# Optimization experiments

Hardware: AMD Instinct MI355X
Metric: run time of the kernel (lower is better)

The kernel has to match this reference:

```python
import jax, jax.numpy as jnp
import numpy as np

DIM = 3072
NUM_HEADS = 24
HEAD_DIM = 128
EPS = 1e-6


def setup_inputs() -> dict:
    key = jax.random.key(0)
    ks = jax.random.split(key, 16)
    B, S_new, S_cached = 2, 256, 8192
    s = 0.02
    return {
        "x": jax.random.normal(ks[0], (B, S_new, DIM), jnp.float32),
        "freqs": jax.random.uniform(ks[1], (S_new, HEAD_DIM // 2), jnp.float32, 0.0, 2 * np.pi),
        "k_cache": jax.random.normal(ks[2], (B, S_cached, DIM), jnp.float32),
        "v_cache": jax.random.normal(ks[3], (B, S_cached, DIM), jnp.float32),
        "Wq": jax.random.normal(ks[4], (DIM, DIM), jnp.float32) * s,
        "bq": jnp.zeros((DIM,), jnp.float32),
        "Wk": jax.random.normal(ks[5], (DIM, DIM), jnp.float32) * s,
        "bk": jnp.zeros((DIM,), jnp.float32),
        "Wv": jax.random.normal(ks[6], (DIM, DIM), jnp.float32) * s,
        "bv": jnp.zeros((DIM,), jnp.float32),
        "Wo": jax.random.normal(ks[7], (DIM, DIM), jnp.float32) * s,
        "bo": jnp.zeros((DIM,), jnp.float32),
        "gq": jnp.ones((DIM,), jnp.float32),
        "gk": jnp.ones((DIM,), jnp.float32),
    }


def _rmsnorm(t, g):
    return t * jax.lax.rsqrt(jnp.mean(t * t, axis=-1, keepdims=True) + EPS) * g


def _rope(t, freqs):
    # t: [B, S, DIM]; freqs: [S, HEAD_DIM//2] angles (complex e^{i*theta} multiply,
    # interleaved-pair layout, matching torch view_as_complex on (..., d//2, 2)).
    B, S, D = t.shape
    th = t.reshape(B, S, NUM_HEADS, HEAD_DIM // 2, 2)
    c = jnp.cos(freqs)[None, :, None, :]
    s = jnp.sin(freqs)[None, :, None, :]
    re = th[..., 0] * c - th[..., 1] * s
    im = th[..., 0] * s + th[..., 1] * c
    return jnp.stack([re, im], axis=-1).reshape(B, S, D)


def reference(x, freqs, k_cache, v_cache, Wq, bq, Wk, bk, Wv, bv, Wo, bo, gq, gk):
    B, S_new, _ = x.shape
    S_cached = k_cache.shape[1]
    S_tot = S_cached + S_new

    q = _rmsnorm(x @ Wq.T + bq, gq)
    k = _rmsnorm(x @ Wk.T + bk, gk)
    v = x @ Wv.T + bv

    q = _rope(q, freqs)
    k = _rope(k, freqs)

    # 'extend' cache mode: concat cached K/V with new K/V
    full_k = jnp.concatenate([k_cache, k], axis=1)
    full_v = jnp.concatenate([v_cache, v], axis=1)

    qh = q.reshape(B, S_new, NUM_HEADS, HEAD_DIM)
    kh = full_k.reshape(B, S_tot, NUM_HEADS, HEAD_DIM)
    vh = full_v.reshape(B, S_tot, NUM_HEADS, HEAD_DIM)

    scale = 1.0 / np.sqrt(HEAD_DIM)
    scores = jnp.einsum("bqhd,bkhd->bhqk", qh, kh) * scale
    probs = jax.nn.softmax(scores, axis=-1)
    out = jnp.einsum("bhqk,bkhd->bqhd", probs, vh).reshape(B, S_new, DIM)
    return out @ Wo.T + bo
```

## Files before the change

kernel.cpp:

```cpp
#include <hip/hip_runtime.h>
#include <hip/hip_bf16.h>

#define NH 24
#define HD 128
#define DM 3072
#define NB 2
#define SN 256
#define MR 512
#define SCACHE 8192
#define NCH 9

typedef float f32x4 __attribute__((ext_vector_type(4)));
typedef float f32x2 __attribute__((ext_vector_type(2)));
typedef short s16x8 __attribute__((ext_vector_type(8)));
typedef short s16x4 __attribute__((ext_vector_type(4)));
typedef unsigned u32x4 __attribute__((ext_vector_type(4)));

__device__ __forceinline__ short bfc(float f) {
    __hip_bfloat16 h = __float2bfloat16(f);
    return __builtin_bit_cast(short, h);
}

__global__ __launch_bounds__(256) void xcast(const float* __restrict__ src, short* __restrict__ dst)
{
    const int i = (blockIdx.x * 256 + threadIdx.x) * 8;
    f32x4 a = *(const f32x4*)(src + i);
    f32x4 b = *(const f32x4*)(src + i + 4);
    s16x8 o;
    #pragma unroll
    for (int j = 0; j < 4; ++j) { o[j] = bfc(a[j]); o[4 + j] = bfc(b[j]); }
    *(s16x8*)(dst + i) = o;
}

__global__ __launch_bounds__(256, 3) void gemm_bias(
    const short* __restrict__ A,
    const float* __restrict__ W0, const float* __restrict__ W1, const float* __restrict__ W2,
    const float* __restrict__ b0, const float* __restrict__ b1, const float* __restrict__ b2,
    float* __restrict__ O0, float* __restrict__ O1, float* __restrict__ O2)
{
    const int z = blockIdx.z;
    const float* W    = (z == 0) ? W0 : (z == 1) ? W1 : W2;
    const float* bias = (z == 0) ? b0 : (z == 1) ? b1 : b2;
    float* O          = (z == 0) ? O0 : (z == 1) ? O1 : O2;

    const int n0 = blockIdx.x * 64;
    const int m0 = blockIdx.y * 128;
    const int t = threadIdx.x;
    const int lane = t & 63;
    const int wave = t >> 6;
    const int l15 = lane & 15, l4 = lane >> 4;
    const int wm = wave * 32;

    __shared__ short As[128][72];
    __shared__ short Bs[64][72];

    f32x4 acc[2][4] = {};
    s16x8 areg[4];
    f32x4 breg[4];

    #pragma unroll
    for (int i = 0; i < 4; ++i) {
        int lin = i * 256 + t;
        areg[i] = *(const s16x8*)(A + (size_t)(m0 + (lin >> 3)) * DM + (lin & 7) * 8);
    }
    #pragma unroll
    for (int i = 0; i < 4; ++i) {
        int lin = i * 256 + t;
        breg[i] = *(const f32x4*)(W + (size_t)(n0 + (lin >> 4)) * DM + (lin & 15) * 4);
    }

    for (int ks = 0; ks < DM / 64; ++ks) {
        #pragma unroll
        for (int i = 0; i < 4; ++i) {
            int lin = i * 256 + t;
            *(s16x8*)&As[lin >> 3][(lin & 7) * 8] = areg[i];
        }
        #pragma unroll
        for (int i = 0; i < 4; ++i) {
            int lin = i * 256 + t;
            s16x4 w4;
            #pragma unroll
            for (int j = 0; j < 4; ++j) w4[j] = bfc(breg[i][j]);
            *(s16x4*)&Bs[lin >> 4][(lin & 15) * 4] = w4;
        }
        __syncthreads();
        if (ks + 1 < DM / 64) {
            int k0 = (ks + 1) * 64;
            #pragma unroll
            for (int i = 0; i < 4; ++i) {
                int lin = i * 256 + t;
                areg[i] = *(const s16x8*)(A + (size_t)(m0 + (lin >> 3)) * DM + k0 + (lin & 7) * 8);
            }
            #pragma unroll
            for (int i = 0; i < 4; ++i) {
                int lin = i * 256 + t;
                breg[i] = *(const f32x4*)(W + (size_t)(n0 + (lin >> 4)) * DM + k0 + (lin & 15) * 4);
            }
        }
        #pragma unroll
        for (int kt = 0; kt < 2; ++kt) {
            s16x8 af[2], bfr[4];
            #pragma unroll
            for (int i = 0; i < 2; ++i)
                af[i]  = *(const s16x8*)&As[wm + i * 16 + l15][kt * 32 + l4 * 8];
            #pragma unroll
            for (int i = 0; i < 4; ++i)
                bfr[i] = *(const s16x8*)&Bs[i * 16 + l15][kt * 32 + l4 * 8];
            #pragma unroll
            for (int mi = 0; mi < 2; ++mi)
                #pragma unroll
                for (int ni = 0; ni < 4; ++ni)
                    acc[mi][ni] = __builtin_amdgcn_mfma_f32_16x16x32_bf16(
                        af[mi], bfr[ni], acc[mi][ni], 0, 0, 0);
        }
        __syncthreads();
    }

    #pragma unroll
    for (int ni = 0; ni < 4; ++ni) {
        int col = n0 + ni * 16 + l15;
        float bv = bias[col];
        #pragma unroll
        for (int mi = 0; mi < 2; ++mi) {
            int row = m0 + wm + mi * 16 + l4 * 4;
            #pragma unroll
            for (int r = 0; r < 4; ++r)
                O[(size_t)(row + r) * DM + col] = acc[mi][ni][r] + bv;
        }
    }
}

__global__ __launch_bounds__(256) void norm_rope(
    float* __restrict__ qf, float* __restrict__ kf, short* __restrict__ qbf,
    const float* __restrict__ gq, const float* __restrict__ gk,
    const float* __restrict__ freqs)
{
    const int buf = blockIdx.x >> 9;
    const int row = blockIdx.x & 511;
    const int t = threadIdx.x;
    float* src = buf ? kf : qf;
    const float* g = buf ? gk : gq;

    f32x2 v[6];
    float ss = 0.f;
    #pragma unroll
    for (int i = 0; i < 6; ++i) {
        int p = t + 256 * i;
        v[i] = *(const f32x2*)(src + (size_t)row * DM + 2 * p);
        ss += v[i][0] * v[i][0] + v[i][1] * v[i][1];
    }
    #pragma unroll
    for (int m = 1; m < 64; m <<= 1) ss += __shfl_xor(ss, m);
    __shared__ float red[4];
    if ((t & 63) == 0) red[t >> 6] = ss;
    __syncthreads();
    ss = red[0] + red[1] + red[2] + red[3];
    const float scale = rsqrtf(ss * (1.0f / DM) + 1e-6f);
    const float QS = 0.08838834764831845f * 1.4426950408889634f;

    const int spos = row & 255;
    #pragma unroll
    for (int i = 0; i < 6; ++i) {
        int p = t + 256 * i;
        int d2 = p & 63;
        float fr = freqs[spos * 64 + d2];
        float snv, cs;
        __sincosf(fr, &snv, &cs);
        f32x2 gg = *(const f32x2*)(g + 2 * p);
        float re = v[i][0] * scale * gg[0];
        float im = v[i][1] * scale * gg[1];
        float re2 = re * cs - im * snv;
        float im2 = re * snv + im * cs;
        if (buf == 0) {
            re2 *= QS; im2 *= QS;
            unsigned pack = (unsigned)(unsigned short)bfc(re2)
                          | ((unsigned)(unsigned short)bfc(im2) << 16);
            *(unsigned*)(qbf + (size_t)row * DM + 2 * p) = pack;
        } else {
            f32x2 o; o[0] = re2; o[1] = im2;
            *(f32x2*)(src + (size_t)row * DM + 2 * p) = o;
        }
    }
}

__global__ __launch_bounds__(512) void attn_fa(
    const short* __restrict__ qbf,
    const float* __restrict__ kf, const float* __restrict__ vf,
    const float* __restrict__ kcache, const float* __restrict__ vcache,
    short* __restrict__ partO, float* __restrict__ partM, float* __restrict__ partL)
{
    const int bid = blockIdx.x;
    const int linear = (bid & 7) * 54 + (bid >> 3);
    const int c  = linear / 48;
    const int bh = linear % 48;
    const int b = bh / NH, h = bh % NH;
    const int t = threadIdx.x, lane = t & 63, wave = t >> 6;
    const int l15 = lane & 15, l4 = lane >> 4;
    const int hoff = h * HD;

    __shared__ short KsA[2][64 * 128];
    __shared__ short VtA[2][128 * 64];

    s16x8 qb[2][4];
    #pragma unroll
    for (int nj = 0; nj < 2; ++nj) {
        int qrow = b * SN + wave * 32 + nj * 16 + l15;
        #pragma unroll
        for (int kt = 0; kt < 4; ++kt)
            qb[nj][kt] = *(const s16x8*)(qbf + (size_t)qrow * DM + hoff + kt * 32 + l4 * 8);
    }

    f32x4 acc[2][8] = {};
    float mrun[2] = {-INFINITY, -INFINITY};
    float lpart[2] = {0.f, 0.f};

    const int ts = (c < 6) ? c * 15 : 90 + (c - 6) * 14;
    const int NT = (c < 6) ? 15 : 14;

    const float* kcB = kcache + (size_t)b * SCACHE * DM + hoff;
    const float* knB = kf     + (size_t)b * SN * DM + hoff;
    const float* vcB = vcache + (size_t)b * SCACHE * DM + hoff;
    const float* vnB = vf     + (size_t)b * SN * DM + hoff;

    auto kaddr = [&](int r, int col) -> const float* {
        return (r < SCACHE) ? (kcB + (size_t)r * DM + col)
                            : (knB + (size_t)(r - SCACHE) * DM + col);
    };
    auto vaddr = [&](int r, int col) -> const float* {
        return (r < SCACHE) ? (vcB + (size_t)r * DM + col)
                            : (vnB + (size_t)(r - SCACHE) * DM + col);
    };

    const int vrow = t & 63, vw = t >> 6;
    f32x4 kreg[4], vreg[4];

    {
        const int kr = ts * 64;
        #pragma unroll
        for (int i = 0; i < 4; ++i) {
            int lin = i * 512 + t;
            kreg[i] = *(const f32x4*)kaddr(kr + (lin >> 5), (lin & 31) * 4);
        }
        #pragma unroll
        for (int j = 0; j < 4; ++j)
            vreg[j] = *(const f32x4*)vaddr(kr + vrow, vw * 16 + j * 4);
    }

    const bool ghi = (l4 & 2) != 0;
    const bool gin = (l4 == 0) || (l4 == 3);

    for (int nt = 0; nt < NT; ++nt) {
        char* KsB = (char*)KsA[nt & 1];
        char* VtB = (char*)VtA[nt & 1];

        #pragma unroll
        for (int i = 0; i < 4; ++i) {
            int lin = i * 512 + t;
            int row = lin >> 5, col4 = lin & 31;
            s16x4 k4;
            #pragma unroll
            for (int j = 0; j < 4; ++j) k4[j] = bfc(kreg[i][j]);
            *(s16x4*)(KsB + (row << 8) + ((((col4 >> 1) ^ row) & 15) << 4) + ((col4 & 1) << 3)) = k4;
        }
        #pragma unroll
        for (int j = 0; j < 4; ++j) {
            #pragma unroll
            for (int jj = 0; jj < 4; ++jj) {
                int d = vw * 16 + j * 4 + jj;
                *(short*)(VtB + (d << 7) + ((((vrow >> 3) ^ (d & 7))) << 4) + ((vrow & 7) << 1)) = bfc(vreg[j][jj]);
            }
        }
        __syncthreads();

        if (nt + 1 < NT) {
            const int kr1 = (ts + nt + 1) * 64;
            #pragma unroll
            for (int i = 0; i < 4; ++i) {
                int lin = i * 512 + t;
                kreg[i] = *(const f32x4*)kaddr(kr1 + (lin >> 5), (lin & 31) * 4);
            }
            #pragma unroll
            for (int j = 0; j < 4; ++j)
                vreg[j] = *(const f32x4*)vaddr(kr1 + vrow, vw * 16 + j * 4);
        }

        f32x4 st[4][2] = {};
        #pragma unroll
        for (int kt = 0; kt < 4; ++kt)
            #pragma unroll
            for (int mi = 0; mi < 4; ++mi) {
                int row = mi * 16 + l15;
                s16x8 kfr = *(const s16x8*)(KsB + (row << 8) + (((kt * 4 + l4) ^ l15) << 4));
                st[mi][0] = __builtin_amdgcn_mfma_f32_16x16x32_bf16(kfr, qb[0][kt], st[mi][0], 0, 0, 0);
                st[mi][1] = __builtin_amdgcn_mfma_f32_16x16x32_bf16(kfr, qb[1][kt], st[mi][1], 0, 0, 0);
            }

        float lx0 = fmaxf(
            fmaxf(fmaxf(fmaxf(st[0][0][0], st[0][0][1]), fmaxf(st[0][0][2], st[0][0][3])),
                  fmaxf(fmaxf(st[1][0][0], st[1][0][1]), fmaxf(st[1][0][2], st[1][0][3]))),
            fmaxf(fmaxf(fmaxf(st[2][0][0], st[2][0][1]), fmaxf(st[2][0][2], st[2][0][3])),
                  fmaxf(fmaxf(st[3][0][0], st[3][0][1]), fmaxf(st[3][0][2], st[3][0][3]))));
        float lx1 = fmaxf(
            fmaxf(fmaxf(fmaxf(st[0][1][0], st[0][1][1]), fmaxf(st[0][1][2], st[0][1][3])),
                  fmaxf(fmaxf(st[1][1][0], st[1][1][1]), fmaxf(st[1][1][2], st[1][1][3]))),
            fmaxf(fmaxf(fmaxf(st[2][1][0], st[2][1][1]), fmaxf(st[2][1][2], st[2][1][3])),
                  fmaxf(fmaxf(st[3][1][0], st[3][1][1]), fmaxf(st[3][1][2], st[3][1][3]))));

        if (!__all((lx0 <= mrun[0] + 8.0f) && (lx1 <= mrun[1] + 8.0f))) {
            float lm0 = fmaxf(lx0, __shfl_xor(lx0, 16)); lm0 = fmaxf(lm0, __shfl_xor(lm0, 32));
            float lm1 = fmaxf(lx1, __shfl_xor(lx1, 16)); lm1 = fmaxf(lm1, __shfl_xor(lm1, 32));
            float mn0 = fmaxf(mrun[0], lm0), mn1 = fmaxf(mrun[1], lm1);
            float c0 = exp2f(mrun[0] - mn0), c1 = exp2f(mrun[1] - mn1);
            mrun[0] = mn0; mrun[1] = mn1;
            lpart[0] *= c0; lpart[1] *= c1;
            #pragma unroll
            for (int df = 0; df < 8; ++df) { acc[0][df] *= c0; acc[1][df] *= c1; }
        }

        #pragma unroll
        for (int mi = 0; mi < 4; ++mi)
            #pragma unroll
            for (int r = 0; r < 4; ++r) {
                float p0 = exp2f(st[mi][0][r] - mrun[0]);
                float p1 = exp2f(st[mi][1][r] - mrun[1]);
                st[mi][0][r] = p0; st[mi][1][r] = p1;
                lpart[0] += p0; lpart[1] += p1;
            }

        unsigned up[2][4][2];
        #pragma unroll
        for (int nj = 0; nj < 2; ++nj)
            #pragma unroll
            for (int mi = 0; mi < 4; ++mi)
                #pragma unroll
                for (int i = 0; i < 2; ++i)
                    up[nj][mi][i] = (unsigned)(unsigned short)bfc(st[mi][nj][2 * i])
                                  | ((unsigned)(unsigned short)bfc(st[mi][nj][2 * i + 1]) << 16);

        s16x8 bp[2][2];
        #pragma unroll
        for (int nj = 0; nj < 2; ++nj)
            #pragma unroll
            for (int kt2 = 0; kt2 < 2; ++kt2) {
                unsigned own0 = ghi ? up[nj][kt2 * 2 + 1][0] : up[nj][kt2 * 2 + 0][0];
                unsigned own1 = ghi ? up[nj][kt2 * 2 + 1][1] : up[nj][kt2 * 2 + 0][1];
                unsigned alt0 = ghi ? up[nj][kt2 * 2 + 0][0] : up[nj][kt2 * 2 + 1][0];
                unsigned alt1 = ghi ? up[nj][kt2 * 2 + 0][1] : up[nj][kt2 * 2 + 1][1];
                unsigned o16_0 = __shfl_xor(own0, 16), o16_1 = __shfl_xor(own1, 16);
                unsigned o32_0 = __shfl_xor(alt0, 32), o32_1 = __shfl_xor(alt1, 32);
                unsigned o48_0 = __shfl_xor(alt0, 48), o48_1 = __shfl_xor(alt1, 48);
                u32x4 uu;
                uu[0] = gin ? (ghi ? o16_0 : own0) : (ghi ? o32_0 : o48_0);
                uu[1] = gin ? (ghi ? o16_1 : own1) : (ghi ? o32_1 : o48_1);
                uu[2] = gin ? (ghi ? own0 : o16_0) : (ghi ? o48_0 : o32_0);
                uu[3] = gin ? (ghi ? own1 : o16_1) : (ghi ? o48_1 : o32_1);
                bp[nj][kt2] = __builtin_bit_cast(s16x8, uu);
            }

        #pragma unroll
        for (int kt2 = 0; kt2 < 2; ++kt2)
            #pragma unroll
            for (int df = 0; df < 8; ++df) {
                int row = df * 16 + l15;
                s16x8 vfr = *(const s16x8*)(VtB + (row << 7) + (((kt2 * 4 + l4) ^ (row & 7)) << 4));
                acc[0][df] = __builtin_amdgcn_mfma_f32_16x16x32_bf16(vfr, bp[0][kt2], acc[0][df], 0, 0, 0);
                acc[1][df] = __builtin_amdgcn_mfma_f32_16x16x32_bf16(vfr, bp[1][kt2], acc[1][df], 0, 0, 0);
            }
    }

    float l0 = lpart[0]; l0 += __shfl_xor(l0, 16); l0 += __shfl_xor(l0, 32);
    float l1 = lpart[1]; l1 += __shfl_xor(l1, 16); l1 += __shfl_xor(l1, 32);

    #pragma unroll
    for (int nj = 0; nj < 2; ++nj) {
        size_t rowid = (size_t)bh * SN + wave * 32 + nj * 16 + l15;
        short* po = partO + (rowid * NCH + c) * HD + l4 * 4;
        #pragma unroll
        for (int df = 0; df < 8; ++df) {
            s16x4 ob;
            #pragma unroll
            for (int r = 0; r < 4; ++r) ob[r] = bfc(acc[nj][df][r]);
            *(s16x4*)(po + df * 16) = ob;
        }
        if (l4 == 0) {
            partM[rowid * NCH + c] = mrun[nj];
            partL[rowid * NCH + c] = (nj == 0) ? l0 : l1;
        }
    }
}

__global__ __launch_bounds__(128) void combine(
    const short* __restrict__ partO, const float* __restrict__ partM,
    const float* __restrict__ partL, short* __restrict__ attnb)
{
    const int rowid = blockIdx.x;
    const int bh = rowid >> 8, q = rowid & 255;
    const int b = bh / NH, h = bh % NH;
    const int d = threadIdx.x;

    float m[NCH];
    float M = -INFINITY;
    #pragma unroll
    for (int c = 0; c < NCH; ++c) { m[c] = partM[(size_t)rowid * NCH + c]; M = fmaxf(M, m[c]); }
    float L = 0.f, o = 0.f;
    #pragma unroll
    for (int c = 0; c < NCH; ++c) {
        float w = exp2f(m[c] - M);
        L += partL[(size_t)rowid * NCH + c] * w;
        unsigned ub = (unsigned)(unsigned short)partO[((size_t)rowid * NCH + c) * HD + d];
        float ov = __builtin_bit_cast(float, ub << 16);
        o += ov * w;
    }
    attnb[(size_t)(b * SN + q) * DM + h * HD + d] = bfc(o / L);
}

extern "C" void kernel_launch(void* const* d_in, const int* in_sizes, int n_in,
                              void* d_out, int out_size, void* d_ws, size_t ws_size,
                              hipStream_t stream) {
    const float* x      = (const float*)d_in[0];
    const float* freqs  = (const float*)d_in[1];
    const float* kcache = (const float*)d_in[2];
    const float* vcache = (const float*)d_in[3];
    const float* Wq = (const float*)d_in[4];
    const float* bq = (const float*)d_in[5];
    const float* Wk = (const float*)d_in[6];
    const float* bk = (const float*)d_in[7];
    const float* Wv = (const float*)d_in[8];
    const float* bv = (const float*)d_in[9];
    const float* Wo = (const float*)d_in[10];
    const float* bo = (const float*)d_in[11];
    const float* gq = (const float*)d_in[12];
    const float* gk = (const float*)d_in[13];
    float* out = (float*)d_out;

    auto al = [](size_t v) { return (v + 255) & ~(size_t)255; };
    const size_t SZ_QF  = (size_t)MR * DM * 4;
    const size_t SZ_QBF = (size_t)MR * DM * 2;
    const size_t SZ_PML = (size_t)48 * SN * NCH * 4;
    const size_t SZ_PO  = (size_t)48 * SN * NCH * HD * 2;

    char* ws = (char*)d_ws;
    float* qf    = (float*)ws; ws += al(SZ_QF);
    float* kfb   = (float*)ws; ws += al(SZ_QF);
    float* vfb   = (float*)ws; ws += al(SZ_QF);
    short* qbf   = (short*)ws; ws += al(SZ_QBF);
    short* xb    = (short*)ws; ws += al(SZ_QBF);
    short* attnb = (short*)ws; ws += al(SZ_QBF);
    float* pM    = (float*)ws; ws += al(SZ_PML);
    float* pL    = (float*)ws; ws += al(SZ_PML);
    short* pO    = (short*)ws; ws += al(SZ_PO);

    xcast<<<dim3(768), 256, 0, stream>>>(x, xb);
    gemm_bias<<<dim3(48, 4, 3), 256, 0, stream>>>(xb, Wq, Wk, Wv, bq, bk, bv, qf, kfb, vfb);
    norm_rope<<<dim3(1024), 256, 0, stream>>>(qf, kfb, qbf, gq, gk, freqs);
    attn_fa<<<dim3(432), 512, 0, stream>>>(qbf, kfb, vfb, kcache, vcache, pO, pM, pL);
    combine<<<dim3(12288), 128, 0, stream>>>(pO, pM, pL, attnb);
    gemm_bias<<<dim3(48, 4, 1), 256, 0, stream>>>(attnb, Wo, Wo, Wo, bo, bo, bo, out, out, out);
}
```

Before: 275.0 us.

## Compute softmax row sums with MFMA against ones and hoist K/V tile base selection

Result: no change. 273.4 us (median of 2 runs) (-0.6%).

```diff
diff --git a/kernel.cpp b/kernel.cpp
--- a/kernel.cpp
+++ b/kernel.cpp
@@ -183,7 +183,7 @@
     }
 }
 
-__global__ __launch_bounds__(512) void attn_fa(
+__global__ __launch_bounds__(512, 2) void attn_fa(
     const short* __restrict__ qbf,
     const float* __restrict__ kf, const float* __restrict__ vf,
     const float* __restrict__ kcache, const float* __restrict__ vcache,
@@ -211,8 +211,12 @@
     }
 
     f32x4 acc[2][8] = {};
+    f32x4 accL[2] = {};
     float mrun[2] = {-INFINITY, -INFINITY};
-    float lpart[2] = {0.f, 0.f};
+
+    s16x8 ones1;
+    #pragma unroll
+    for (int j = 0; j < 8; ++j) ones1[j] = (short)0x3F80;
 
     const int ts = (c < 6) ? c * 15 : 90 + (c - 6) * 14;
     const int NT = (c < 6) ? 15 : 14;
@@ -222,28 +226,22 @@
     const float* vcB = vcache + (size_t)b * SCACHE * DM + hoff;
     const float* vnB = vf     + (size_t)b * SN * DM + hoff;
 
-    auto kaddr = [&](int r, int col) -> const float* {
-        return (r < SCACHE) ? (kcB + (size_t)r * DM + col)
-                            : (knB + (size_t)(r - SCACHE) * DM + col);
-    };
-    auto vaddr = [&](int r, int col) -> const float* {
-        return (r < SCACHE) ? (vcB + (size_t)r * DM + col)
-                            : (vnB + (size_t)(r - SCACHE) * DM + col);
-    };
-
     const int vrow = t & 63, vw = t >> 6;
     f32x4 kreg[4], vreg[4];
 
     {
         const int kr = ts * 64;
+        const float* kb; const float* vb;
+        if (kr < SCACHE) { kb = kcB + (size_t)kr * DM; vb = vcB + (size_t)kr * DM; }
+        else             { kb = knB + (size_t)(kr - SCACHE) * DM; vb = vnB + (size_t)(kr - SCACHE) * DM; }
         #pragma unroll
         for (int i = 0; i < 4; ++i) {
             int lin = i * 512 + t;
-            kreg[i] = *(const f32x4*)kaddr(kr + (lin >> 5), (lin & 31) * 4);
+            kreg[i] = *(const f32x4*)(kb + (size_t)(lin >> 5) * DM + (lin & 31) * 4);
         }
         #pragma unroll
         for (int j = 0; j < 4; ++j)
-            vreg[j] = *(const f32x4*)vaddr(kr + vrow, vw * 16 + j * 4);
+            vreg[j] = *(const f32x4*)(vb + (size_t)vrow * DM + vw * 16 + j * 4);
     }
 
     const bool ghi = (l4 & 2) != 0;
@@ -274,14 +272,17 @@
 
         if (nt + 1 < NT) {
             const int kr1 = (ts + nt + 1) * 64;
+            const float* kb; const float* vb;
+            if (kr1 < SCACHE) { kb = kcB + (size_t)kr1 * DM; vb = vcB + (size_t)kr1 * DM; }
+            else              { kb = knB + (size_t)(kr1 - SCACHE) * DM; vb = vnB + (size_t)(kr1 - SCACHE) * DM; }
             #pragma unroll
             for (int i = 0; i < 4; ++i) {
                 int lin = i * 512 + t;
-                kreg[i] = *(const f32x4*)kaddr(kr1 + (lin >> 5), (lin & 31) * 4);
+                kreg[i] = *(const f32x4*)(kb + (size_t)(lin >> 5) * DM + (lin & 31) * 4);
             }
             #pragma unroll
             for (int j = 0; j < 4; ++j)
-                vreg[j] = *(const f32x4*)vaddr(kr1 + vrow, vw * 16 + j * 4);
+                vreg[j] = *(const f32x4*)(vb + (size_t)vrow * DM + vw * 16 + j * 4);
         }
 
         f32x4 st[4][2] = {};
@@ -295,16 +296,18 @@
                 st[mi][1] = __builtin_amdgcn_mfma_f32_16x16x32_bf16(kfr, qb[1][kt], st[mi][1], 0, 0, 0);
             }
 
-        float lx0 = fmaxf(
-            fmaxf(fmaxf(fmaxf(st[0][0][0], st[0][0][1]), fmaxf(st[0][0][2], st[0][0][3])),
-                  fmaxf(fmaxf(st[1][0][0], st[1][0][1]), fmaxf(st[1][0][2], st[1][0][3]))),
-            fmaxf(fmaxf(fmaxf(st[2][0][0], st[2][0][1]), fmaxf(st[2][0][2], st[2][0][3])),
-                  fmaxf(fmaxf(st[3][0][0], st[3][0][1]), fmaxf(st[3][0][2], st[3][0][3]))));
-        float lx1 = fmaxf(
-            fmaxf(fmaxf(fmaxf(st[0][1][0], st[0][1][1]), fmaxf(st[0][1][2], st[0][1][3])),
-                  fmaxf(fmaxf(st[1][1][0], st[1][1][1]), fmaxf(st[1][1][2], st[1][1][3]))),
-            fmaxf(fmaxf(fmaxf(st[2][1][0], st[2][1][1]), fmaxf(st[2][1][2], st[2][1][3])),
-                  fmaxf(fmaxf(st[3][1][0], st[3][1][1]), fmaxf(st[3][1][2], st[3][1][3]))));
+        float a0 = fmaxf(fmaxf(st[0][0][0], st[0][0][1]), st[0][0][2]);
+        float a1 = fmaxf(fmaxf(st[0][0][3], st[1][0][0]), st[1][0][1]);
+        float a2 = fmaxf(fmaxf(st[1][0][2], st[1][0][3]), st[2][0][0]);
+        float a3 = fmaxf(fmaxf(st[2][0][1], st[2][0][2]), st[2][0][3]);
+        float a4 = fmaxf(fmaxf(st[3][0][0], st[3][0][1]), st[3][0][2]);
+        float lx0 = fmaxf(fmaxf(fmaxf(a0, a1), a2), fmaxf(fmaxf(a3, a4), st[3][0][3]));
+        float b0_ = fmaxf(fmaxf(st[0][1][0], st[0][1][1]), st[0][1][2]);
+        float b1_ = fmaxf(fmaxf(st[0][1][3], st[1][1][0]), st[1][1][1]);
+        float b2_ = fmaxf(fmaxf(st[1][1][2], st[1][1][3]), st[2][1][0]);
+        float b3_ = fmaxf(fmaxf(st[2][1][1], st[2][1][2]), st[2][1][3]);
+        float b4_ = fmaxf(fmaxf(st[3][1][0], st[3][1][1]), st[3][1][2]);
+        float lx1 = fmaxf(fmaxf(fmaxf(b0_, b1_), b2_), fmaxf(fmaxf(b3_, b4_), st[3][1][3]));
 
         if (!__all((lx0 <= mrun[0] + 8.0f) && (lx1 <= mrun[1] + 8.0f))) {
             float lm0 = fmaxf(lx0, __shfl_xor(lx0, 16)); lm0 = fmaxf(lm0, __shfl_xor(lm0, 32));
@@ -312,7 +315,7 @@
             float mn0 = fmaxf(mrun[0], lm0), mn1 = fmaxf(mrun[1], lm1);
             float c0 = exp2f(mrun[0] - mn0), c1 = exp2f(mrun[1] - mn1);
             mrun[0] = mn0; mrun[1] = mn1;
-            lpart[0] *= c0; lpart[1] *= c1;
+            accL[0] *= c0; accL[1] *= c1;
             #pragma unroll
             for (int df = 0; df < 8; ++df) { acc[0][df] *= c0; acc[1][df] *= c1; }
         }
@@ -321,10 +324,8 @@
         for (int mi = 0; mi < 4; ++mi)
             #pragma unroll
             for (int r = 0; r < 4; ++r) {
-                float p0 = exp2f(st[mi][0][r] - mrun[0]);
-                float p1 = exp2f(st[mi][1][r] - mrun[1]);
-                st[mi][0][r] = p0; st[mi][1][r] = p1;
-                lpart[0] += p0; lpart[1] += p1;
+                st[mi][0][r] = exp2f(st[mi][0][r] - mrun[0]);
+                st[mi][1][r] = exp2f(st[mi][1][r] - mrun[1]);
             }
 
         unsigned up[2][4][2];
@@ -358,7 +359,7 @@
             }
 
         #pragma unroll
-        for (int kt2 = 0; kt2 < 2; ++kt2)
+        for (int kt2 = 0; kt2 < 2; ++kt2) {
             #pragma unroll
             for (int df = 0; df < 8; ++df) {
                 int row = df * 16 + l15;
@@ -366,10 +367,10 @@
                 acc[0][df] = __builtin_amdgcn_mfma_f32_16x16x32_bf16(vfr, bp[0][kt2], acc[0][df], 0, 0, 0);
                 acc[1][df] = __builtin_amdgcn_mfma_f32_16x16x32_bf16(vfr, bp[1][kt2], acc[1][df], 0, 0, 0);
             }
-    }
-
-    float l0 = lpart[0]; l0 += __shfl_xor(l0, 16); l0 += __shfl_xor(l0, 32);
-    float l1 = lpart[1]; l1 += __shfl_xor(l1, 16); l1 += __shfl_xor(l1, 32);
+            accL[0] = __builtin_amdgcn_mfma_f32_16x16x32_bf16(ones1, bp[0][kt2], accL[0], 0, 0, 0);
+            accL[1] = __builtin_amdgcn_mfma_f32_16x16x32_bf16(ones1, bp[1][kt2], accL[1], 0, 0, 0);
+        }
+    }
 
     #pragma unroll
     for (int nj = 0; nj < 2; ++nj) {
@@ -384,7 +385,7 @@
         }
         if (l4 == 0) {
             partM[rowid * NCH + c] = mrun[nj];
-            partL[rowid * NCH + c] = (nj == 0) ? l0 : l1;
+            partL[rowid * NCH + c] = accL[nj][0];
         }
     }
 }
```
